# Kernel optimization log

Hardware: AMD Instinct MI355X
Metric: run time of the kernel (lower is better)

The kernel has to match this reference:

```python
import jax, jax.numpy as jnp
import numpy as np

SEARCH_SIZE = 21
BLOCK_SIZE = 4


def _inter_prediction(im1, im2, search_size=SEARCH_SIZE, block_size=BLOCK_SIZE):
    # im1, im2: [B, 1, H, W]; returns [B, 1, H, W]
    B, C, H, W = im1.shape
    p = search_size // 2
    s2 = search_size * search_size
    im2_pad = jnp.pad(im2, ((0, 0), (0, 0), (p, p), (p, p)))
    # All SxS shifted views of im2, stacked on channel dim: [B, S^2, H, W].
    # Channel k = (i, j) row-major corresponds to im2_pad[:, :, i:i+H, j:j+W],
    # matching the torch double loop (note: output is permutation-invariant
    # over shifts anyway since weights are derived from the same tensor).
    nbr = jax.lax.conv_general_dilated_patches(
        im2_pad, (search_size, search_size), (1, 1), 'VALID')
    diff = jnp.abs(im1 - nbr)  # broadcast [B,1,H,W] against [B,S^2,H,W]
    h, w = H // block_size, W // block_size
    # avg_pool2d with kernel=stride=block_size via reshape-mean
    vol = diff.reshape(B, s2, h, block_size, w, block_size).mean(axis=(3, 5))
    idx = jax.nn.softmax(-100.0 * vol, axis=1)  # [B, S^2, h, w]
    # repeat_interleave(block_size) along both spatial dims
    idx_full = jnp.broadcast_to(
        idx[:, :, :, None, :, None],
        (B, s2, h, block_size, w, block_size)).reshape(B, s2, H, W)
    return jnp.sum(idx_full * nbr, axis=1, keepdims=True)


def setup_inputs() -> dict:
    key = jax.random.key(0)
    k1, k2 = jax.random.split(key)
    im1 = jax.random.normal(k1, (2, 1, 256, 256), dtype=jnp.float32)
    im2 = jax.random.normal(k2, (2, 1, 256, 256), dtype=jnp.float32)
    return {"im1": im1, "im2": im2}


def reference(im1, im2):
    return _inter_prediction(im1, im2)
```

## Files before the change

### kernel.cpp

```cpp
#include <hip/hip_runtime.h>
#include <math.h>


#define HH 256
#define WW 256
#define SSZ 21
#define PAD 10
#define NSH 441
#define WIN 28

__global__ __launch_bounds__(256) void pred_kernel(
    const float* __restrict__ im1, const float* __restrict__ im2,
    float* __restrict__ out) {
  __shared__ float win[WIN * WIN];

  const int tid = threadIdx.x;
  const int T = blockIdx.x;
  const int b = T >> 10;
  const int rem = T & 1023;
  const int tr = rem >> 5;
  const int tc = rem & 31;
  const float* im2b = im2 + b * (HH * WW);

  for (int e = tid; e < WIN * WIN; e += 256) {
    int wr = e / WIN;
    int wc = e - wr * WIN;
    int gr = tr * 8 + wr - PAD;
    int gc = tc * 8 + wc - PAD;
    float v = 0.f;
    if ((unsigned)gr < HH && (unsigned)gc < WW) v = im2b[gr * WW + gc];
    win[e] = v;
  }
  __syncthreads();

  const int wave = tid >> 6;
  const int lane = tid & 63;
  const int by = tr * 2 + (wave >> 1);
  const int bx = tc * 2 + (wave & 1);
  const int wbase = ((wave >> 1) * 4) * WIN + (wave & 1) * 4;

  float a[16];
  const float* im1b = im1 + b * (HH * WW) + (by * 4) * WW + bx * 4;
#pragma unroll
  for (int dy = 0; dy < 4; ++dy) {
    const float4 r = *reinterpret_cast<const float4*>(im1b + dy * WW);
    a[dy * 4 + 0] = r.x; a[dy * 4 + 1] = r.y;
    a[dy * 4 + 2] = r.z; a[dy * 4 + 3] = r.w;
  }

  const float cc = 9.016844005556021f;
  float m = 1e30f, l = 0.f;
  float o[16];
#pragma unroll
  for (int t = 0; t < 16; ++t) o[t] = 0.f;

  int i = lane / 21;
  int j = lane - i * 21;
  for (int k = lane; k < NSH; k += 64) {
    const float* wp = &win[wbase + i * WIN + j];
    float wv[16];
#pragma unroll
    for (int dy = 0; dy < 4; ++dy)
#pragma unroll
      for (int dx = 0; dx < 4; ++dx) wv[dy * 4 + dx] = wp[dy * WIN + dx];

    float s0 = 0.f, s1 = 0.f, s2 = 0.f, s3 = 0.f;
#pragma unroll
    for (int dy = 0; dy < 4; ++dy) {
      s0 += fabsf(a[dy * 4 + 0] - wv[dy * 4 + 0]);
      s1 += fabsf(a[dy * 4 + 1] - wv[dy * 4 + 1]);
      s2 += fabsf(a[dy * 4 + 2] - wv[dy * 4 + 2]);
      s3 += fabsf(a[dy * 4 + 3] - wv[dy * 4 + 3]);
    }
    const float v = (s0 + s1) + (s2 + s3);

    const float mn = fminf(m, v);
    const float beta = __builtin_amdgcn_exp2f(cc * (mn - m));
    const float p = __builtin_amdgcn_exp2f(cc * (mn - v));
    m = mn;
    l = l * beta + p;
#pragma unroll
    for (int t = 0; t < 16; ++t) o[t] = __builtin_fmaf(o[t], beta, p * wv[t]);

    j += 1; i += 3;
    if (j >= 21) { j -= 21; i += 1; }
  }

  const float lm = m;
#pragma unroll
  for (int off = 32; off; off >>= 1) m = fminf(m, __shfl_xor(m, off, 64));
  const float beta = __builtin_amdgcn_exp2f(cc * (m - lm));
  l *= beta;
#pragma unroll
  for (int t = 0; t < 16; ++t) o[t] *= beta;
#pragma unroll
  for (int off = 32; off; off >>= 1) {
    l += __shfl_xor(l, off, 64);
#pragma unroll
    for (int t = 0; t < 16; ++t) o[t] += __shfl_xor(o[t], off, 64);
  }

  const float rinv = __builtin_amdgcn_rcpf(l);
  if (lane == 0) {
    float* op = out + b * (HH * WW) + (by * 4) * WW + bx * 4;
#pragma unroll
    for (int dy = 0; dy < 4; ++dy) {
      float4 v4 = make_float4(o[dy * 4 + 0] * rinv, o[dy * 4 + 1] * rinv,
                              o[dy * 4 + 2] * rinv, o[dy * 4 + 3] * rinv);
      *reinterpret_cast<float4*>(op + dy * WW) = v4;
    }
  }
}

extern "C" void kernel_launch(void* const* d_in, const int* in_sizes, int n_in,
                              void* d_out, int out_size, void* d_ws, size_t ws_size,
                              hipStream_t stream) {
  const float* im1 = (const float*)d_in[0];
  const float* im2 = (const float*)d_in[1];
  float* out = (float*)d_out;
  const int B = in_sizes[0] / (HH * WW);
  pred_kernel<<<B * 1024, 256, 0, stream>>>(im1, im2, out);
}
```

Measured before the change: 71.75 us.

## Assign each lane a row of seven shifts with register-reused window and transpose reduction

New measurement: 65.33 us. 1.1x faster.

```diff
diff --git a/kernel.cpp b/kernel.cpp
--- a/kernel.cpp
+++ b/kernel.cpp
@@ -4,15 +4,15 @@
 
 #define HH 256
 #define WW 256
-#define SSZ 21
 #define PAD 10
-#define NSH 441
-#define WIN 28
+#define WINR 28
+#define WSTR 29
+#define LDSN (WINR * WSTR)
 
 __global__ __launch_bounds__(256) void pred_kernel(
     const float* __restrict__ im1, const float* __restrict__ im2,
     float* __restrict__ out) {
-  __shared__ float win[WIN * WIN];
+  __shared__ float win[LDSN];
 
   const int tid = threadIdx.x;
   const int T = blockIdx.x;
@@ -22,9 +22,9 @@
   const int tc = rem & 31;
   const float* im2b = im2 + b * (HH * WW);
 
-  for (int e = tid; e < WIN * WIN; e += 256) {
-    int wr = e / WIN;
-    int wc = e - wr * WIN;
+  for (int e = tid; e < LDSN; e += 256) {
+    int wr = e / WSTR;
+    int wc = e - wr * WSTR;
     int gr = tr * 8 + wr - PAD;
     int gc = tc * 8 + wc - PAD;
     float v = 0.f;
@@ -37,7 +37,7 @@
   const int lane = tid & 63;
   const int by = tr * 2 + (wave >> 1);
   const int bx = tc * 2 + (wave & 1);
-  const int wbase = ((wave >> 1) * 4) * WIN + (wave & 1) * 4;
+  const int wbase = ((wave >> 1) * 4) * WSTR + (wave & 1) * 4;
 
   float a[16];
   const float* im1b = im1 + b * (HH * WW) + (by * 4) * WW + bx * 4;
@@ -48,67 +48,103 @@
     a[dy * 4 + 2] = r.z; a[dy * 4 + 3] = r.w;
   }
 
+  const int i = lane / 3;
+  const int j0 = (lane - i * 3) * 7;
+  const int base = wbase + i * WSTR + j0;
+  float w[40];
+#pragma unroll
+  for (int dy = 0; dy < 4; ++dy)
+#pragma unroll
+    for (int c = 0; c < 10; ++c) w[dy * 10 + c] = win[base + dy * WSTR + c];
+
+  float sad[7];
+#pragma unroll
+  for (int t = 0; t < 7; ++t) {
+    float s0 = 0.f, s1 = 0.f, s2 = 0.f, s3 = 0.f;
+#pragma unroll
+    for (int dy = 0; dy < 4; ++dy) {
+      s0 += fabsf(a[dy * 4 + 0] - w[dy * 10 + t + 0]);
+      s1 += fabsf(a[dy * 4 + 1] - w[dy * 10 + t + 1]);
+      s2 += fabsf(a[dy * 4 + 2] - w[dy * 10 + t + 2]);
+      s3 += fabsf(a[dy * 4 + 3] - w[dy * 10 + t + 3]);
+    }
+    sad[t] = (s0 + s1) + (s2 + s3);
+  }
+  if (lane == 63) {
+#pragma unroll
+    for (int t = 0; t < 7; ++t) sad[t] = 3.0e38f;
+  }
+
+  float m = sad[0];
+#pragma unroll
+  for (int t = 1; t < 7; ++t) m = fminf(m, sad[t]);
+#pragma unroll
+  for (int off = 32; off; off >>= 1) m = fminf(m, __shfl_xor(m, off, 64));
+
   const float cc = 9.016844005556021f;
-  float m = 1e30f, l = 0.f;
+  float l = 0.f;
   float o[16];
 #pragma unroll
   for (int t = 0; t < 16; ++t) o[t] = 0.f;
-
-  int i = lane / 21;
-  int j = lane - i * 21;
-  for (int k = lane; k < NSH; k += 64) {
-    const float* wp = &win[wbase + i * WIN + j];
-    float wv[16];
+#pragma unroll
+  for (int t = 0; t < 7; ++t) {
+    const float p = __builtin_amdgcn_exp2f(cc * (m - sad[t]));
+    l += p;
 #pragma unroll
     for (int dy = 0; dy < 4; ++dy)
 #pragma unroll
-      for (int dx = 0; dx < 4; ++dx) wv[dy * 4 + dx] = wp[dy * WIN + dx];
-
-    float s0 = 0.f, s1 = 0.f, s2 = 0.f, s3 = 0.f;
-#pragma unroll
-    for (int dy = 0; dy < 4; ++dy) {
-      s0 += fabsf(a[dy * 4 + 0] - wv[dy * 4 + 0]);
-      s1 += fabsf(a[dy * 4 + 1] - wv[dy * 4 + 1]);
-      s2 += fabsf(a[dy * 4 + 2] - wv[dy * 4 + 2]);
-      s3 += fabsf(a[dy * 4 + 3] - wv[dy * 4 + 3]);
-    }
-    const float v = (s0 + s1) + (s2 + s3);
-
-    const float mn = fminf(m, v);
-    const float beta = __builtin_amdgcn_exp2f(cc * (mn - m));
-    const float p = __builtin_amdgcn_exp2f(cc * (mn - v));
-    m = mn;
-    l = l * beta + p;
-#pragma unroll
-    for (int t = 0; t < 16; ++t) o[t] = __builtin_fmaf(o[t], beta, p * wv[t]);
-
-    j += 1; i += 3;
-    if (j >= 21) { j -= 21; i += 1; }
+      for (int dx = 0; dx < 4; ++dx)
+        o[dy * 4 + dx] = __builtin_fmaf(p, w[dy * 10 + t + dx], o[dy * 4 + dx]);
   }
 
-  const float lm = m;
+  float r8[8];
+  {
+    const bool up = (lane & 32) != 0;
 #pragma unroll
-  for (int off = 32; off; off >>= 1) m = fminf(m, __shfl_xor(m, off, 64));
-  const float beta = __builtin_amdgcn_exp2f(cc * (m - lm));
-  l *= beta;
+    for (int q = 0; q < 8; ++q) {
+      const float send = up ? o[q] : o[q + 8];
+      const float recv = __shfl_xor(send, 32, 64);
+      r8[q] = (up ? o[q + 8] : o[q]) + recv;
+    }
+  }
+  float r4[4];
+  {
+    const bool up = (lane & 16) != 0;
 #pragma unroll
-  for (int t = 0; t < 16; ++t) o[t] *= beta;
+    for (int q = 0; q < 4; ++q) {
+      const float send = up ? r8[q] : r8[q + 4];
+      const float recv = __shfl_xor(send, 16, 64);
+      r4[q] = (up ? r8[q + 4] : r8[q]) + recv;
+    }
+  }
+  float r2[2];
+  {
+    const bool up = (lane & 8) != 0;
 #pragma unroll
-  for (int off = 32; off; off >>= 1) {
-    l += __shfl_xor(l, off, 64);
+    for (int q = 0; q < 2; ++q) {
+      const float send = up ? r4[q] : r4[q + 2];
+      const float recv = __shfl_xor(send, 8, 64);
+      r2[q] = (up ? r4[q + 2] : r4[q]) + recv;
+    }
+  }
+  float r1;
+  {
+    const bool up = (lane & 4) != 0;
+    const float send = up ? r2[0] : r2[1];
+    const float recv = __shfl_xor(send, 4, 64);
+    r1 = (up ? r2[1] : r2[0]) + recv;
+  }
+  r1 += __shfl_xor(r1, 2, 64);
+  r1 += __shfl_xor(r1, 1, 64);
+
 #pragma unroll
-    for (int t = 0; t < 16; ++t) o[t] += __shfl_xor(o[t], off, 64);
-  }
+  for (int off = 32; off; off >>= 1) l += __shfl_xor(l, off, 64);
+  const float rinv = __builtin_amdgcn_rcpf(l);
 
-  const float rinv = __builtin_amdgcn_rcpf(l);
-  if (lane == 0) {
-    float* op = out + b * (HH * WW) + (by * 4) * WW + bx * 4;
-#pragma unroll
-    for (int dy = 0; dy < 4; ++dy) {
-      float4 v4 = make_float4(o[dy * 4 + 0] * rinv, o[dy * 4 + 1] * rinv,
-                              o[dy * 4 + 2] * rinv, o[dy * 4 + 3] * rinv);
-      *reinterpret_cast<float4*>(op + dy * WW) = v4;
-    }
+  if ((lane & 3) == 0) {
+    const int t = lane >> 2;
+    out[b * (HH * WW) + (by * 4 + (t >> 2)) * WW + bx * 4 + (t & 3)] =
+        r1 * rinv;
   }
 }
 
```
